# Kernel optimization log

Measured on AMD Instinct MI355X. Metric: run time of the kernel, lower is better.

## Reference

```python
import jax, jax.numpy as jnp
import numpy as np

N = 50000      # nodes
E = 800000     # edges
F_IN = 256     # input node features
H = 64         # hidden_dim
C = 10         # num_classes
G = 64         # graphs in batch


def setup_inputs() -> dict:
    key = jax.random.key(0)
    ks = jax.random.split(key, 10)
    x = jax.random.normal(ks[0], (N, F_IN), dtype=jnp.float32)
    edge_index = jax.random.randint(ks[1], (2, E), 0, N, dtype=jnp.int64)
    batch = jnp.sort(jax.random.randint(ks[2], (N,), 0, G, dtype=jnp.int64))
    def glorot(k, fan_in, fan_out):
        return jax.random.normal(k, (fan_in, fan_out), dtype=jnp.float32) / jnp.sqrt(jnp.float32(fan_in))
    return {
        "x": x,
        "edge_index": edge_index,
        "batch": batch,
        "W1": glorot(ks[3], F_IN, H), "b1": jnp.zeros((H,), jnp.float32),
        "W2": glorot(ks[4], H, H),    "b2": jnp.zeros((H,), jnp.float32),
        "W3": glorot(ks[5], H, H),    "b3": jnp.zeros((H,), jnp.float32),
        "lin_W": glorot(ks[6], H, C), "lin_b": jnp.zeros((C,), jnp.float32),
    }


def reference(x, edge_index, batch, W1, b1, W2, b2, W3, b3, lin_W, lin_b):
    src, dst = edge_index[0], edge_index[1]
    # GCN normalization with self-loops: deg counts (A + I) in-degree
    deg = jax.ops.segment_sum(jnp.ones((E,), x.dtype), dst, num_segments=N) + 1.0
    dis = jax.lax.rsqrt(deg)                       # deg^{-1/2}, [N]
    edge_norm = dis[src] * dis[dst]                # [E]
    self_norm = dis * dis                          # [N] (self-loop weight)

    def gcn_conv_relu(h, W, b):
        h = h @ W                                  # [N, H]
        msg = h[src] * edge_norm[:, None]          # gather + scale, [E, H]
        agg = jax.ops.segment_sum(msg, dst, num_segments=N)
        agg = agg + h * self_norm[:, None]         # self-loop contribution
        return jax.nn.relu(agg + b)                # dropout is identity in eval

    h = gcn_conv_relu(x, W1, b1)
    h = gcn_conv_relu(h, W2, b2)
    h = gcn_conv_relu(h, W3, b3)

    # global mean pool over graphs
    counts = jax.ops.segment_sum(jnp.ones((N,), h.dtype), batch, num_segments=G)
    pooled = jax.ops.segment_sum(h, batch, num_segments=G) / jnp.maximum(counts, 1.0)[:, None]
    return pooled @ lin_W + lin_b                  # [G, C]
```

## Files before the change

### kernel.cpp

```cpp
#include <hip/hip_runtime.h>

#define N_NODES 50000
#define N_EDGES 800000
#define F_INPUT 256
#define HDIM 64
#define NCLS 10
#define NGRAPH 64

#define BSHIFT 7
#define NBUCK 391
#define SCAP 4096

typedef float f32x4v __attribute__((ext_vector_type(4)));
typedef short bf16x8 __attribute__((ext_vector_type(8)));

union B8U { uint4 q; bf16x8 v; };

__device__ __forceinline__ float bflo(unsigned v) { return __uint_as_float(v << 16); }
__device__ __forceinline__ float bfhi(unsigned v) { return __uint_as_float(v & 0xFFFF0000u); }
__device__ __forceinline__ unsigned f2b2(float a, float b) {
    unsigned x = __float_as_uint(a); x = (x + 0x7FFF + ((x >> 16) & 1)) >> 16;
    unsigned y = __float_as_uint(b); y = (y + 0x7FFF + ((y >> 16) & 1)) >> 16;
    return x | (y << 16);
}

__device__ __forceinline__ void split2(float x0, float x1, unsigned& h, unsigned& l) {
    unsigned u0 = __float_as_uint(x0), u1 = __float_as_uint(x1);
    unsigned m0 = u0 & 0xFFFF0000u, m1 = u1 & 0xFFFF0000u;
    h = (u0 >> 16) | m1;
    float r0 = x0 - __uint_as_float(m0);
    float r1 = x1 - __uint_as_float(m1);
    l = (__float_as_uint(r0) >> 16) | (__float_as_uint(r1) & 0xFFFF0000u);
}

#define ADD8(b, u)                                    \
    b##0 += bflo(u.x); b##1 += bfhi(u.x);             \
    b##2 += bflo(u.y); b##3 += bfhi(u.y);             \
    b##4 += bflo(u.z); b##5 += bfhi(u.z);             \
    b##6 += bflo(u.w); b##7 += bfhi(u.w);

__global__ __launch_bounds__(256) void k_part(const int* __restrict__ src,
                                              const int* __restrict__ dst,
                                              int* __restrict__ bcnt,
                                              int* __restrict__ stage, int E) {
    __shared__ int cnt[NBUCK];
    __shared__ int base[NBUCK];
    const int tid = threadIdx.x;
    const int e0 = blockIdx.x * 4096;
    int pb[16], pv[16];
    for (int t = tid; t < NBUCK; t += 256) cnt[t] = 0;
    __syncthreads();
#pragma unroll
    for (int j = 0; j < 16; ++j) {
        int e = e0 + j * 256 + tid;
        if (e < E) {
            int s = src[e], d = dst[e];
            pb[j] = d >> BSHIFT;
            pv[j] = (s << BSHIFT) | (d & 127);
            atomicAdd(&cnt[pb[j]], 1);
        } else pb[j] = -1;
    }
    __syncthreads();
    for (int t = tid; t < NBUCK; t += 256) {
        int c = cnt[t];
        base[t] = c ? atomicAdd(&bcnt[t], c) : 0;
        cnt[t] = 0;
    }
    __syncthreads();
#pragma unroll
    for (int j = 0; j < 16; ++j) {
        if (pb[j] >= 0) {
            int r = base[pb[j]] + atomicAdd(&cnt[pb[j]], 1);
            if (r < SCAP) stage[pb[j] * SCAP + r] = pv[j];
        }
    }
}

__global__ __launch_bounds__(256) void k_csr(const int* __restrict__ stage,
                                             const int* __restrict__ bcnt,
                                             float* __restrict__ dis,
                                             int4* __restrict__ rng,
                                             int* __restrict__ eadj, int n) {
    __shared__ int cnt[128];
    __shared__ int loc[128];
    __shared__ int lcur[128];
    __shared__ int ebuf[SCAP];
    const int b = blockIdx.x;
    const int tid = threadIdx.x;
    const int n0 = b << BSHIFT;
    const int nn = min(128, n - n0);
    const int sb = b * SCAP;
    const int len = min(bcnt[b], SCAP);
    if (tid < 128) cnt[tid] = 0;
    __syncthreads();
    for (int j = tid; j < len; j += 256) atomicAdd(&cnt[stage[sb + j] & 127], 1);
    __syncthreads();
    if (tid < 128) loc[tid] = cnt[tid];
    __syncthreads();
    for (int d = 1; d < 128; d <<= 1) {
        int x = 0;
        if (tid < 128 && tid >= d) x = loc[tid - d];
        __syncthreads();
        if (tid < 128) loc[tid] += x;
        __syncthreads();
    }
    if (tid < 128) {
        int ex = loc[tid] - cnt[tid];
        if (tid < nn) {
            int dg = cnt[tid];
            float di = rsqrtf((float)(dg + 1));
            dis[n0 + tid] = di;
            rng[n0 + tid] = make_int4(sb + ex, sb + ex + dg, __float_as_int(di), 0);
        }
        lcur[tid] = ex;
    }
    __syncthreads();
    for (int j = tid; j < len; j += 256) {
        int p = stage[sb + j];
        int rk = atomicAdd(&lcur[p & 127], 1);
        ebuf[rk] = p >> BSHIFT;
    }
    __syncthreads();
    for (int j = tid; j < len; j += 256) eadj[sb + j] = ebuf[j];
}

__global__ __launch_bounds__(256) void k_prepZ(const float* __restrict__ W1,
                                               const float* __restrict__ W2,
                                               const float* __restrict__ W3,
                                               uint4* __restrict__ Bf1,
                                               uint4* __restrict__ Bf2,
                                               uint4* __restrict__ Bf3,
                                               int* __restrict__ bcnt,
                                               float* __restrict__ pooled) {
    int s = blockIdx.x * 256 + threadIdx.x;
    for (int j = s; j < NBUCK; j += 3072) bcnt[j] = 0;
    for (int j = s; j < NGRAPH * HDIM; j += 3072) pooled[j] = 0.f;
    const float* W; uint4* out; int local, KS;
    if (s < 2048)      { W = W1; out = Bf1; local = s;        KS = 8; }
    else if (s < 2560) { W = W2; out = Bf2; local = s - 2048; KS = 2; }
    else               { W = W3; out = Bf3; local = s - 2560; KS = 2; }
    const int lane = local & 63;
    const int t    = (local >> 6) & 3;
    const int ks   = local >> 8;
    const int kb   = ks * 32 + ((lane >> 4) << 3);
    const int col  = t * 16 + (lane & 15);
    unsigned h[4], l[4];
#pragma unroll
    for (int j = 0; j < 4; ++j) {
        float x0 = W[(size_t)(kb + 2 * j) * HDIM + col];
        float x1 = W[(size_t)(kb + 2 * j + 1) * HDIM + col];
        split2(x0, x1, h[j], l[j]);
    }
    out[(ks * 4 + t) * 64 + lane]          = make_uint4(h[0], h[1], h[2], h[3]);
    out[((KS + ks) * 4 + t) * 64 + lane]   = make_uint4(l[0], l[1], l[2], l[3]);
}

__global__ __launch_bounds__(256) void k_gemm_mf(const float* __restrict__ A,
                                                 const uint4* __restrict__ Bf,
                                                 const float* __restrict__ dis,
                                                 unsigned short* __restrict__ C,
                                                 int n, int lda, int ktn) {
    const int tid = threadIdx.x;
    const int ln  = tid & 63;
    const int wv  = tid >> 6;
    const int m   = ln & 15;
    const int kg  = ln >> 4;
    const int grow = blockIdx.x * 64 + wv * 16 + m;
    const float* ar = A + (size_t)min(grow, n - 1) * lda + kg * 8;

    f32x4v acc[4];
#pragma unroll
    for (int t = 0; t < 4; ++t)
#pragma unroll
        for (int j = 0; j < 4; ++j) acc[t][j] = 0.0f;

    float4 c0 = *(const float4*)(ar);
    float4 c1 = *(const float4*)(ar + 4);

    for (int ks = 0; ks < ktn; ++ks) {
        const int kn = (ks + 1 < ktn) ? (ks + 1) * 32 : 0;
        float4 p0 = *(const float4*)(ar + kn);
        float4 p1 = *(const float4*)(ar + kn + 4);

        const uint4* bp = Bf + (size_t)ks * 256 + ln;
        const uint4* bq = Bf + (size_t)(ktn + ks) * 256 + ln;
        B8U bh0, bh1, bh2, bh3, bl0, bl1, bl2, bl3;
        bh0.q = bp[0];   bh1.q = bp[64];  bh2.q = bp[128]; bh3.q = bp[192];
        bl0.q = bq[0];   bl1.q = bq[64];  bl2.q = bq[128]; bl3.q = bq[192];

        B8U ah, al;
        split2(c0.x, c0.y, ah.q.x, al.q.x);
        split2(c0.z, c0.w, ah.q.y, al.q.y);
        split2(c1.x, c1.y, ah.q.z, al.q.z);
        split2(c1.z, c1.w, ah.q.w, al.q.w);

        acc[0] = __builtin_amdgcn_mfma_f32_16x16x32_bf16(bh0.v, ah.v, acc[0], 0, 0, 0);
        acc[1] = __builtin_amdgcn_mfma_f32_16x16x32_bf16(bh1.v, ah.v, acc[1], 0, 0, 0);
        acc[2] = __builtin_amdgcn_mfma_f32_16x16x32_bf16(bh2.v, ah.v, acc[2], 0, 0, 0);
        acc[3] = __builtin_amdgcn_mfma_f32_16x16x32_bf16(bh3.v, ah.v, acc[3], 0, 0, 0);
        acc[0] = __builtin_amdgcn_mfma_f32_16x16x32_bf16(bl0.v, ah.v, acc[0], 0, 0, 0);
        acc[1] = __builtin_amdgcn_mfma_f32_16x16x32_bf16(bl1.v, ah.v, acc[1], 0, 0, 0);
        acc[2] = __builtin_amdgcn_mfma_f32_16x16x32_bf16(bl2.v, ah.v, acc[2], 0, 0, 0);
        acc[3] = __builtin_amdgcn_mfma_f32_16x16x32_bf16(bl3.v, ah.v, acc[3], 0, 0, 0);
        acc[0] = __builtin_amdgcn_mfma_f32_16x16x32_bf16(bh0.v, al.v, acc[0], 0, 0, 0);
        acc[1] = __builtin_amdgcn_mfma_f32_16x16x32_bf16(bh1.v, al.v, acc[1], 0, 0, 0);
        acc[2] = __builtin_amdgcn_mfma_f32_16x16x32_bf16(bh2.v, al.v, acc[2], 0, 0, 0);
        acc[3] = __builtin_amdgcn_mfma_f32_16x16x32_bf16(bh3.v, al.v, acc[3], 0, 0, 0);

        c0 = p0; c1 = p1;
    }

    if (grow < n) {
        const float di = dis[grow];
#pragma unroll
        for (int t = 0; t < 4; ++t) {
            uint2 p;
            p.x = f2b2(acc[t][0] * di, acc[t][1] * di);
            p.y = f2b2(acc[t][2] * di, acc[t][3] * di);
            *(uint2*)(C + (size_t)grow * HDIM + t * 16 + kg * 4) = p;
        }
    }
}

__global__ __launch_bounds__(256) void k_fgg(const unsigned short* __restrict__ h,
                                             const int* __restrict__ eadj,
                                             const int4* __restrict__ rng,
                                             const float* __restrict__ bias,
                                             const uint4* __restrict__ Bf,
                                             const float* __restrict__ dis,
                                             unsigned short* __restrict__ out, int n) {
    __shared__ uint4 rl[32 * 8];
    const int tid = threadIdx.x;
    const int i0 = blockIdx.x * 32;
    const int node = tid >> 3;
    const int l8 = tid & 7;
    const int i = i0 + node;
    uint4 o = make_uint4(0u, 0u, 0u, 0u);
    if (i < n) {
        const int q = l8 * 8;
        const int4 r = rng[i];
        int e = r.x; const int e1 = r.y;
        const float di = __int_as_float(r.z);
        float a0 = 0.f, a1 = 0.f, a2 = 0.f, a3 = 0.f, a4 = 0.f, a5 = 0.f, a6 = 0.f, a7 = 0.f;
        float g0 = 0.f, g1 = 0.f, g2 = 0.f, g3 = 0.f, g4 = 0.f, g5 = 0.f, g6 = 0.f, g7 = 0.f;
#pragma unroll 2
        for (; e + 3 < e1; e += 4) {
            int s0 = eadj[e];
            int s1 = eadj[e + 1];
            int s2 = eadj[e + 2];
            int s3 = eadj[e + 3];
            uint4 u0 = *(const uint4*)(h + (size_t)s0 * HDIM + q);
            uint4 u1 = *(const uint4*)(h + (size_t)s1 * HDIM + q);
            uint4 u2 = *(const uint4*)(h + (size_t)s2 * HDIM + q);
            uint4 u3 = *(const uint4*)(h + (size_t)s3 * HDIM + q);
            ADD8(a, u0)
            ADD8(g, u1)
            ADD8(a, u2)
            ADD8(g, u3)
        }
        for (; e < e1; ++e) {
            int s0 = eadj[e];
            uint4 u0 = *(const uint4*)(h + (size_t)s0 * HDIM + q);
            ADD8(a, u0)
        }
        uint4 us = *(const uint4*)(h + (size_t)i * HDIM + q);
        ADD8(a, us)
        a0 += g0; a1 += g1; a2 += g2; a3 += g3;
        a4 += g4; a5 += g5; a6 += g6; a7 += g7;
        float4 bl = *(const float4*)(bias + q);
        float4 bh = *(const float4*)(bias + q + 4);
        a0 = fmaxf(fmaf(a0, di, bl.x), 0.f);
        a1 = fmaxf(fmaf(a1, di, bl.y), 0.f);
        a2 = fmaxf(fmaf(a2, di, bl.z), 0.f);
        a3 = fmaxf(fmaf(a3, di, bl.w), 0.f);
        a4 = fmaxf(fmaf(a4, di, bh.x), 0.f);
        a5 = fmaxf(fmaf(a5, di, bh.y), 0.f);
        a6 = fmaxf(fmaf(a6, di, bh.z), 0.f);
        a7 = fmaxf(fmaf(a7, di, bh.w), 0.f);
        o.x = f2b2(a0, a1); o.y = f2b2(a2, a3);
        o.z = f2b2(a4, a5); o.w = f2b2(a6, a7);
    }
    rl[node * 8 + (l8 ^ (node & 7))] = o;
    __syncthreads();

    const int ln = tid & 63;
    const int wv = tid >> 6;
    const int m  = ln & 15;
    const int kg = ln >> 4;
    const int row = (wv >> 1) * 16 + m;
    const int ct0 = (wv & 1) * 2;
    f32x4v acc0, acc1;
#pragma unroll
    for (int j = 0; j < 4; ++j) { acc0[j] = 0.f; acc1[j] = 0.f; }
#pragma unroll
    for (int ks = 0; ks < 2; ++ks) {
        B8U af;
        af.q = rl[row * 8 + ((ks * 4 + kg) ^ (row & 7))];
        const uint4* bp = Bf + ks * 256 + ln;
        const uint4* bq = Bf + (2 + ks) * 256 + ln;
        B8U bh0, bh1, bl0, bl1;
        bh0.q = bp[ct0 * 64]; bh1.q = bp[(ct0 + 1) * 64];
        bl0.q = bq[ct0 * 64]; bl1.q = bq[(ct0 + 1) * 64];
        acc0 = __builtin_amdgcn_mfma_f32_16x16x32_bf16(bh0.v, af.v, acc0, 0, 0, 0);
        acc1 = __builtin_amdgcn_mfma_f32_16x16x32_bf16(bh1.v, af.v, acc1, 0, 0, 0);
        acc0 = __builtin_amdgcn_mfma_f32_16x16x32_bf16(bl0.v, af.v, acc0, 0, 0, 0);
        acc1 = __builtin_amdgcn_mfma_f32_16x16x32_bf16(bl1.v, af.v, acc1, 0, 0, 0);
    }
    const int grow = i0 + row;
    if (grow < n) {
        const float di = dis[grow];
        uint2 p;
        p.x = f2b2(acc0[0] * di, acc0[1] * di);
        p.y = f2b2(acc0[2] * di, acc0[3] * di);
        *(uint2*)(out + (size_t)grow * HDIM + ct0 * 16 + kg * 4) = p;
        p.x = f2b2(acc1[0] * di, acc1[1] * di);
        p.y = f2b2(acc1[2] * di, acc1[3] * di);
        *(uint2*)(out + (size_t)grow * HDIM + (ct0 + 1) * 16 + kg * 4) = p;
    }
}

__global__ __launch_bounds__(256) void k_gather_pool(const unsigned short* __restrict__ h,
                                                     const int* __restrict__ eadj,
                                                     const int4* __restrict__ rng,
                                                     const float* __restrict__ bias,
                                                     const int* __restrict__ batch,
                                                     float* __restrict__ pooled, int n) {
    __shared__ float sp[NGRAPH][HDIM];
    const int tid = threadIdx.x;
    int t = blockIdx.x * 256 + tid;
    int i = t >> 3;
    const bool valid = (i < n);
    int q = (t & 7) * 8;
    const int i0 = (blockIdx.x * 256) >> 3;
    const int i1 = min(i0 + 32, n);
    const int gmin = batch[min(i0, n - 1)];
    const int gmax = batch[i1 - 1];
    for (int j = tid; j < NGRAPH * HDIM; j += 256) ((float*)sp)[j] = 0.f;
    __syncthreads();
    if (valid) {
        const int4 r = rng[i];
        int e = r.x; const int e1 = r.y;
        const float di = __int_as_float(r.z);
        float a0 = 0.f, a1 = 0.f, a2 = 0.f, a3 = 0.f, a4 = 0.f, a5 = 0.f, a6 = 0.f, a7 = 0.f;
        float g0 = 0.f, g1 = 0.f, g2 = 0.f, g3 = 0.f, g4 = 0.f, g5 = 0.f, g6 = 0.f, g7 = 0.f;
#pragma unroll 2
        for (; e + 3 < e1; e += 4) {
            int s0 = eadj[e];
            int s1 = eadj[e + 1];
            int s2 = eadj[e + 2];
            int s3 = eadj[e + 3];
            uint4 u0 = *(const uint4*)(h + (size_t)s0 * HDIM + q);
            uint4 u1 = *(const uint4*)(h + (size_t)s1 * HDIM + q);
            uint4 u2 = *(const uint4*)(h + (size_t)s2 * HDIM + q);
            uint4 u3 = *(const uint4*)(h + (size_t)s3 * HDIM + q);
            ADD8(a, u0)
            ADD8(g, u1)
            ADD8(a, u2)
            ADD8(g, u3)
        }
        for (; e < e1; ++e) {
            int s0 = eadj[e];
            uint4 u0 = *(const uint4*)(h + (size_t)s0 * HDIM + q);
            ADD8(a, u0)
        }
        uint4 us = *(const uint4*)(h + (size_t)i * HDIM + q);
        ADD8(a, us)
        a0 += g0; a1 += g1; a2 += g2; a3 += g3;
        a4 += g4; a5 += g5; a6 += g6; a7 += g7;
        float4 bl = *(const float4*)(bias + q);
        float4 bh = *(const float4*)(bias + q + 4);
        a0 = fmaxf(fmaf(a0, di, bl.x), 0.f);
        a1 = fmaxf(fmaf(a1, di, bl.y), 0.f);
        a2 = fmaxf(fmaf(a2, di, bl.z), 0.f);
        a3 = fmaxf(fmaf(a3, di, bl.w), 0.f);
        a4 = fmaxf(fmaf(a4, di, bh.x), 0.f);
        a5 = fmaxf(fmaf(a5, di, bh.y), 0.f);
        a6 = fmaxf(fmaf(a6, di, bh.z), 0.f);
        a7 = fmaxf(fmaf(a7, di, bh.w), 0.f);
        int g = batch[i];
        atomicAdd(&sp[g][q + 0], a0); atomicAdd(&sp[g][q + 1], a1);
        atomicAdd(&sp[g][q + 2], a2); atomicAdd(&sp[g][q + 3], a3);
        atomicAdd(&sp[g][q + 4], a4); atomicAdd(&sp[g][q + 5], a5);
        atomicAdd(&sp[g][q + 6], a6); atomicAdd(&sp[g][q + 7], a7);
    }
    __syncthreads();
    int rows = gmax - gmin + 1;
    for (int j = tid; j < rows * HDIM; j += 256) {
        int r = j >> 6, c = j & 63;
        float v = sp[gmin + r][c];
        if (v != 0.f) atomicAdd(&pooled[(gmin + r) * HDIM + c], v);
    }
}

__global__ __launch_bounds__(640) void k_head(const float* __restrict__ pooled,
                                              const int* __restrict__ batch,
                                              const float* __restrict__ linW,
                                              const float* __restrict__ linb,
                                              float* __restrict__ out, int n) {
    int t = threadIdx.x;
    if (t >= NGRAPH * NCLS) return;
    int g = t / NCLS;
    int c = t - g * NCLS;
    int lo = 0, hi = n;
    while (lo < hi) { int m = (lo + hi) >> 1; if (batch[m] < g) lo = m + 1; else hi = m; }
    int s = lo;
    lo = 0; hi = n;
    while (lo < hi) { int m = (lo + hi) >> 1; if (batch[m] < g + 1) lo = m + 1; else hi = m; }
    float inv = 1.0f / fmaxf((float)(lo - s), 1.0f);
    float acc = linb[c];
#pragma unroll
    for (int k = 0; k < HDIM; ++k)
        acc = fmaf(pooled[g * HDIM + k] * inv, linW[k * NCLS + c], acc);
    out[g * NCLS + c] = acc;
}

extern "C" void kernel_launch(void* const* d_in, const int* in_sizes, int n_in,
                              void* d_out, int out_size, void* d_ws, size_t ws_size,
                              hipStream_t stream) {
    (void)in_sizes; (void)n_in; (void)out_size; (void)ws_size;
    const float* x    = (const float*)d_in[0];
    const int*   ei   = (const int*)d_in[1];
    const int*   batch= (const int*)d_in[2];
    const float* W1   = (const float*)d_in[3];
    const float* b1   = (const float*)d_in[4];
    const float* W2   = (const float*)d_in[5];
    const float* b2   = (const float*)d_in[6];
    const float* W3   = (const float*)d_in[7];
    const float* b3   = (const float*)d_in[8];
    const float* linW = (const float*)d_in[9];
    const float* linb = (const float*)d_in[10];
    float* out = (float*)d_out;

    const int N = N_NODES, E = N_EDGES;
    const int* src = ei;
    const int* dst = ei + E;

    char* ws = (char*)d_ws;
    unsigned short* hA = (unsigned short*)ws; ws += (size_t)N * HDIM * 2;
    unsigned short* hB = (unsigned short*)ws; ws += (size_t)N * HDIM * 2;
    float* dis    = (float*)ws; ws += (size_t)N * 4;
    int*   eadj   = (int*)ws;   ws += (size_t)NBUCK * SCAP * 4;
    int*   stage  = (int*)ws;   ws += (size_t)NBUCK * SCAP * 4;
    int4*  rng    = (int4*)ws;  ws += (size_t)N * 16;
    int*   bcnt   = (int*)ws;   ws += ((size_t)NBUCK * 4 + 15) & ~(size_t)15;
    float* pooled = (float*)ws; ws += (size_t)NGRAPH * HDIM * 4;
    uint4* Bf1    = (uint4*)ws; ws += (size_t)2 * 8 * 4 * 64 * 16;
    uint4* Bf2    = (uint4*)ws; ws += (size_t)2 * 2 * 4 * 64 * 16;
    uint4* Bf3    = (uint4*)ws; ws += (size_t)2 * 2 * 4 * 64 * 16;

    const int nbE = (E + 4095) / 4096;
    const int gb  = (N + 63) / 64;
    const int nF  = (N + 31) / 32;

    k_prepZ<<<12, 256, 0, stream>>>(W1, W2, W3, Bf1, Bf2, Bf3, bcnt, pooled);
    k_part<<<nbE, 256, 0, stream>>>(src, dst, bcnt, stage, E);
    k_csr<<<NBUCK, 256, 0, stream>>>(stage, bcnt, dis, rng, eadj, N);

    k_gemm_mf<<<gb, 256, 0, stream>>>(x, Bf1, dis, hA, N, F_INPUT, 8);
    k_fgg<<<nF, 256, 0, stream>>>(hA, eadj, rng, b1, Bf2, dis, hB, N);
    k_fgg<<<nF, 256, 0, stream>>>(hB, eadj, rng, b2, Bf3, dis, hA, N);
    k_gather_pool<<<nF, 256, 0, stream>>>(hA, eadj, rng, b3, batch, pooled, N);
    k_head<<<1, 640, 0, stream>>>(pooled, batch, linW, linb, out, N);
}
```

Baseline: 226.9 us.

## Fuse pipeline into cooperative persistent megakernel and overlap partition with first GEMM

```diff
diff --git a/kernel.cpp b/kernel.cpp
--- a/kernel.cpp
+++ b/kernel.cpp
@@ -1,4 +1,7 @@
 #include <hip/hip_runtime.h>
+#include <hip/hip_cooperative_groups.h>
+
+namespace cg = cooperative_groups;
 
 #define N_NODES 50000
 #define N_EDGES 800000
@@ -10,6 +13,7 @@
 #define BSHIFT 7
 #define NBUCK 391
 #define SCAP 4096
+#define PARTB 196
 
 typedef float f32x4v __attribute__((ext_vector_type(4)));
 typedef short bf16x8 __attribute__((ext_vector_type(8)));
@@ -39,106 +43,39 @@
     b##4 += bflo(u.z); b##5 += bfhi(u.z);             \
     b##6 += bflo(u.w); b##7 += bfhi(u.w);
 
-__global__ __launch_bounds__(256) void k_part(const int* __restrict__ src,
-                                              const int* __restrict__ dst,
-                                              int* __restrict__ bcnt,
-                                              int* __restrict__ stage, int E) {
-    __shared__ int cnt[NBUCK];
-    __shared__ int base[NBUCK];
-    const int tid = threadIdx.x;
-    const int e0 = blockIdx.x * 4096;
-    int pb[16], pv[16];
-    for (int t = tid; t < NBUCK; t += 256) cnt[t] = 0;
-    __syncthreads();
-#pragma unroll
-    for (int j = 0; j < 16; ++j) {
-        int e = e0 + j * 256 + tid;
-        if (e < E) {
-            int s = src[e], d = dst[e];
-            pb[j] = d >> BSHIFT;
-            pv[j] = (s << BSHIFT) | (d & 127);
-            atomicAdd(&cnt[pb[j]], 1);
-        } else pb[j] = -1;
-    }
-    __syncthreads();
-    for (int t = tid; t < NBUCK; t += 256) {
-        int c = cnt[t];
-        base[t] = c ? atomicAdd(&bcnt[t], c) : 0;
-        cnt[t] = 0;
-    }
-    __syncthreads();
-#pragma unroll
-    for (int j = 0; j < 16; ++j) {
-        if (pb[j] >= 0) {
-            int r = base[pb[j]] + atomicAdd(&cnt[pb[j]], 1);
-            if (r < SCAP) stage[pb[j] * SCAP + r] = pv[j];
-        }
-    }
-}
-
-__global__ __launch_bounds__(256) void k_csr(const int* __restrict__ stage,
-                                             const int* __restrict__ bcnt,
-                                             float* __restrict__ dis,
-                                             int4* __restrict__ rng,
-                                             int* __restrict__ eadj, int n) {
-    __shared__ int cnt[128];
-    __shared__ int loc[128];
-    __shared__ int lcur[128];
-    __shared__ int ebuf[SCAP];
-    const int b = blockIdx.x;
-    const int tid = threadIdx.x;
-    const int n0 = b << BSHIFT;
-    const int nn = min(128, n - n0);
-    const int sb = b * SCAP;
-    const int len = min(bcnt[b], SCAP);
-    if (tid < 128) cnt[tid] = 0;
-    __syncthreads();
-    for (int j = tid; j < len; j += 256) atomicAdd(&cnt[stage[sb + j] & 127], 1);
-    __syncthreads();
-    if (tid < 128) loc[tid] = cnt[tid];
-    __syncthreads();
-    for (int d = 1; d < 128; d <<= 1) {
-        int x = 0;
-        if (tid < 128 && tid >= d) x = loc[tid - d];
-        __syncthreads();
-        if (tid < 128) loc[tid] += x;
-        __syncthreads();
-    }
-    if (tid < 128) {
-        int ex = loc[tid] - cnt[tid];
-        if (tid < nn) {
-            int dg = cnt[tid];
-            float di = rsqrtf((float)(dg + 1));
-            dis[n0 + tid] = di;
-            rng[n0 + tid] = make_int4(sb + ex, sb + ex + dg, __float_as_int(di), 0);
-        }
-        lcur[tid] = ex;
-    }
-    __syncthreads();
-    for (int j = tid; j < len; j += 256) {
-        int p = stage[sb + j];
-        int rk = atomicAdd(&lcur[p & 127], 1);
-        ebuf[rk] = p >> BSHIFT;
-    }
-    __syncthreads();
-    for (int j = tid; j < len; j += 256) eadj[sb + j] = ebuf[j];
-}
-
-__global__ __launch_bounds__(256) void k_prepZ(const float* __restrict__ W1,
-                                               const float* __restrict__ W2,
-                                               const float* __restrict__ W3,
-                                               uint4* __restrict__ Bf1,
-                                               uint4* __restrict__ Bf2,
-                                               uint4* __restrict__ Bf3,
-                                               int* __restrict__ bcnt,
-                                               float* __restrict__ pooled) {
-    int s = blockIdx.x * 256 + threadIdx.x;
-    for (int j = s; j < NBUCK; j += 3072) bcnt[j] = 0;
-    for (int j = s; j < NGRAPH * HDIM; j += 3072) pooled[j] = 0.f;
+#define FMA8(b, u, wt)                                                  \
+    b##0 = fmaf(bflo(u.x), wt, b##0); b##1 = fmaf(bfhi(u.x), wt, b##1); \
+    b##2 = fmaf(bflo(u.y), wt, b##2); b##3 = fmaf(bfhi(u.y), wt, b##3); \
+    b##4 = fmaf(bflo(u.z), wt, b##4); b##5 = fmaf(bfhi(u.z), wt, b##5); \
+    b##6 = fmaf(bflo(u.w), wt, b##6); b##7 = fmaf(bfhi(u.w), wt, b##7);
+
+struct MegaP {
+    const int* src; const int* dst; int E; int n;
+    const float* x;
+    const float* W1; const float* W2; const float* W3;
+    const float* b1; const float* b2; const float* b3;
+    const float* linW; const float* linb;
+    const int* batch; float* out;
+    unsigned short* hA; unsigned short* hB;
+    float* dis; int* eadj; int* stage; int4* rng; int* bcnt; float* pooled;
+    uint4* Bf1; uint4* Bf2; uint4* Bf3;
+};
+
+union ShU {
+    struct { int cnt[NBUCK]; int base[NBUCK]; } pt;
+    struct { int cnt[128]; int loc[128]; int lcur[128]; int ebuf[SCAP]; } cs;
+    uint4 rl[256];
+    float sp[NGRAPH][HDIM];
+};
+
+static __device__ void prep_unit(int u, const MegaP& p) {
+    int s = u * 256 + (int)threadIdx.x;
+    for (int j = s; j < NBUCK; j += 3072) p.bcnt[j] = 0;
+    for (int j = s; j < NGRAPH * HDIM; j += 3072) p.pooled[j] = 0.f;
     const float* W; uint4* out; int local, KS;
-    if (s < 2048)      { W = W1; out = Bf1; local = s;        KS = 8; }
-    else if (s < 2560) { W = W2; out = Bf2; local = s - 2048; KS = 2; }
-    else               { W = W3; out = Bf3; local = s - 2560; KS = 2; }
+    if (s < 2048)      { W = p.W1; out = p.Bf1; local = s;        KS = 8; }
+    else if (s < 2560) { W = p.W2; out = p.Bf2; local = s - 2048; KS = 2; }
+    else               { W = p.W3; out = p.Bf3; local = s - 2560; KS = 2; }
     const int lane = local & 63;
     const int t    = (local >> 6) & 3;
     const int ks   = local >> 8;
@@ -151,22 +88,53 @@
         float x1 = W[(size_t)(kb + 2 * j + 1) * HDIM + col];
         split2(x0, x1, h[j], l[j]);
     }
-    out[(ks * 4 + t) * 64 + lane]          = make_uint4(h[0], h[1], h[2], h[3]);
-    out[((KS + ks) * 4 + t) * 64 + lane]   = make_uint4(l[0], l[1], l[2], l[3]);
-}
-
-__global__ __launch_bounds__(256) void k_gemm_mf(const float* __restrict__ A,
-                                                 const uint4* __restrict__ Bf,
-                                                 const float* __restrict__ dis,
-                                                 unsigned short* __restrict__ C,
-                                                 int n, int lda, int ktn) {
+    out[(ks * 4 + t) * 64 + lane]        = make_uint4(h[0], h[1], h[2], h[3]);
+    out[((KS + ks) * 4 + t) * 64 + lane] = make_uint4(l[0], l[1], l[2], l[3]);
+}
+
+static __device__ void part_unit(int u, const MegaP& p, ShU& sh) {
+    const int tid = threadIdx.x;
+    __syncthreads();
+    const int e0 = u * 4096;
+    int pb[16], pv[16];
+    for (int t = tid; t < NBUCK; t += 256) sh.pt.cnt[t] = 0;
+    __syncthreads();
+#pragma unroll
+    for (int j = 0; j < 16; ++j) {
+        int e = e0 + j * 256 + tid;
+        if (e < p.E) {
+            int s = p.src[e], d = p.dst[e];
+            pb[j] = d >> BSHIFT;
+            pv[j] = (s << BSHIFT) | (d & 127);
+            atomicAdd(&sh.pt.cnt[pb[j]], 1);
+        } else pb[j] = -1;
+    }
+    __syncthreads();
+    for (int t = tid; t < NBUCK; t += 256) {
+        int c = sh.pt.cnt[t];
+        sh.pt.base[t] = c ? atomicAdd(&p.bcnt[t], c) : 0;
+        sh.pt.cnt[t] = 0;
+    }
+    __syncthreads();
+#pragma unroll
+    for (int j = 0; j < 16; ++j) {
+        if (pb[j] >= 0) {
+            int r = sh.pt.base[pb[j]] + atomicAdd(&sh.pt.cnt[pb[j]], 1);
+            if (r < SCAP) p.stage[pb[j] * SCAP + r] = pv[j];
+        }
+    }
+}
+
+static __device__ void gemm1_unit(int u, const MegaP& p) {
     const int tid = threadIdx.x;
     const int ln  = tid & 63;
     const int wv  = tid >> 6;
     const int m   = ln & 15;
     const int kg  = ln >> 4;
-    const int grow = blockIdx.x * 64 + wv * 16 + m;
-    const float* ar = A + (size_t)min(grow, n - 1) * lda + kg * 8;
+    const int n   = p.n;
+    const int ktn = 8;
+    const int grow = u * 64 + wv * 16 + m;
+    const float* ar = p.x + (size_t)min(grow, n - 1) * F_INPUT + kg * 8;
 
     f32x4v acc[4];
 #pragma unroll
@@ -182,8 +150,8 @@
         float4 p0 = *(const float4*)(ar + kn);
         float4 p1 = *(const float4*)(ar + kn + 4);
 
-        const uint4* bp = Bf + (size_t)ks * 256 + ln;
-        const uint4* bq = Bf + (size_t)(ktn + ks) * 256 + ln;
+        const uint4* bp = p.Bf1 + (size_t)ks * 256 + ln;
+        const uint4* bq = p.Bf1 + (size_t)(ktn + ks) * 256 + ln;
         B8U bh0, bh1, bh2, bh3, bl0, bl1, bl2, bl3;
         bh0.q = bp[0];   bh1.q = bp[64];  bh2.q = bp[128]; bh3.q = bp[192];
         bl0.q = bq[0];   bl1.q = bq[64];  bl2.q = bq[128]; bl3.q = bq[192];
@@ -211,64 +179,196 @@
     }
 
     if (grow < n) {
-        const float di = dis[grow];
 #pragma unroll
         for (int t = 0; t < 4; ++t) {
-            uint2 p;
-            p.x = f2b2(acc[t][0] * di, acc[t][1] * di);
-            p.y = f2b2(acc[t][2] * di, acc[t][3] * di);
-            *(uint2*)(C + (size_t)grow * HDIM + t * 16 + kg * 4) = p;
-        }
-    }
-}
-
-__global__ __launch_bounds__(256) void k_fgg(const unsigned short* __restrict__ h,
-                                             const int* __restrict__ eadj,
-                                             const int4* __restrict__ rng,
-                                             const float* __restrict__ bias,
-                                             const uint4* __restrict__ Bf,
-                                             const float* __restrict__ dis,
-                                             unsigned short* __restrict__ out, int n) {
-    __shared__ uint4 rl[32 * 8];
-    const int tid = threadIdx.x;
-    const int i0 = blockIdx.x * 32;
+            uint2 pk;
+            pk.x = f2b2(acc[t][0], acc[t][1]);
+            pk.y = f2b2(acc[t][2], acc[t][3]);
+            *(uint2*)(p.hA + (size_t)grow * HDIM + t * 16 + kg * 4) = pk;
+        }
+    }
+}
+
+static __device__ void csr_unit(int u, const MegaP& p, ShU& sh) {
+    const int tid = threadIdx.x;
+    __syncthreads();
+    const int n0 = u << BSHIFT;
+    const int nn = min(128, p.n - n0);
+    const int sb = u * SCAP;
+    const int len = min(p.bcnt[u], SCAP);
+    if (tid < 128) sh.cs.cnt[tid] = 0;
+    __syncthreads();
+    for (int j = tid; j < len; j += 256) atomicAdd(&sh.cs.cnt[p.stage[sb + j] & 127], 1);
+    __syncthreads();
+    if (tid < 128) sh.cs.loc[tid] = sh.cs.cnt[tid];
+    __syncthreads();
+    for (int d = 1; d < 128; d <<= 1) {
+        int x = 0;
+        if (tid < 128 && tid >= d) x = sh.cs.loc[tid - d];
+        __syncthreads();
+        if (tid < 128) sh.cs.loc[tid] += x;
+        __syncthreads();
+    }
+    if (tid < 128) {
+        int ex = sh.cs.loc[tid] - sh.cs.cnt[tid];
+        if (tid < nn) {
+            int dg = sh.cs.cnt[tid];
+            float di = rsqrtf((float)(dg + 1));
+            p.dis[n0 + tid] = di;
+            p.rng[n0 + tid] = make_int4(sb + ex, sb + ex + dg, __float_as_int(di), 0);
+        }
+        sh.cs.lcur[tid] = ex;
+    }
+    __syncthreads();
+    for (int j = tid; j < len; j += 256) {
+        int pv = p.stage[sb + j];
+        int rk = atomicAdd(&sh.cs.lcur[pv & 127], 1);
+        sh.cs.ebuf[rk] = pv >> BSHIFT;
+    }
+    __syncthreads();
+    for (int j = tid; j < len; j += 256) p.eadj[sb + j] = sh.cs.ebuf[j];
+}
+
+static __device__ __forceinline__ void fgg_gemm_tail(const MegaP& p, ShU& sh,
+                                                     const uint4* Bf,
+                                                     unsigned short* out, int i0) {
+    const int tid = threadIdx.x;
+    const int ln = tid & 63;
+    const int wv = tid >> 6;
+    const int m  = ln & 15;
+    const int kg = ln >> 4;
+    const int row = (wv >> 1) * 16 + m;
+    const int ct0 = (wv & 1) * 2;
+    f32x4v acc0, acc1;
+#pragma unroll
+    for (int j = 0; j < 4; ++j) { acc0[j] = 0.f; acc1[j] = 0.f; }
+#pragma unroll
+    for (int ks = 0; ks < 2; ++ks) {
+        B8U af;
+        af.q = sh.rl[row * 8 + ((ks * 4 + kg) ^ (row & 7))];
+        const uint4* bp = Bf + ks * 256 + ln;
+        const uint4* bq = Bf + (2 + ks) * 256 + ln;
+        B8U bh0, bh1, bl0, bl1;
+        bh0.q = bp[ct0 * 64]; bh1.q = bp[(ct0 + 1) * 64];
+        bl0.q = bq[ct0 * 64]; bl1.q = bq[(ct0 + 1) * 64];
+        acc0 = __builtin_amdgcn_mfma_f32_16x16x32_bf16(bh0.v, af.v, acc0, 0, 0, 0);
+        acc1 = __builtin_amdgcn_mfma_f32_16x16x32_bf16(bh1.v, af.v, acc1, 0, 0, 0);
+        acc0 = __builtin_amdgcn_mfma_f32_16x16x32_bf16(bl0.v, af.v, acc0, 0, 0, 0);
+        acc1 = __builtin_amdgcn_mfma_f32_16x16x32_bf16(bl1.v, af.v, acc1, 0, 0, 0);
+    }
+    const int grow = i0 + row;
+    if (grow < p.n) {
+        const float di = p.dis[grow];
+        uint2 pk;
+        pk.x = f2b2(acc0[0] * di, acc0[1] * di);
+        pk.y = f2b2(acc0[2] * di, acc0[3] * di);
+        *(uint2*)(out + (size_t)grow * HDIM + ct0 * 16 + kg * 4) = pk;
+        pk.x = f2b2(acc1[0] * di, acc1[1] * di);
+        pk.y = f2b2(acc1[2] * di, acc1[3] * di);
+        *(uint2*)(out + (size_t)grow * HDIM + (ct0 + 1) * 16 + kg * 4) = pk;
+    }
+}
+
+static __device__ void fggw_unit(int u, const MegaP& p, ShU& sh) {
+    const int tid = threadIdx.x;
+    __syncthreads();
+    const int i0 = u * 32;
     const int node = tid >> 3;
     const int l8 = tid & 7;
     const int i = i0 + node;
     uint4 o = make_uint4(0u, 0u, 0u, 0u);
-    if (i < n) {
+    if (i < p.n) {
         const int q = l8 * 8;
-        const int4 r = rng[i];
+        const int4 r = p.rng[i];
         int e = r.x; const int e1 = r.y;
         const float di = __int_as_float(r.z);
         float a0 = 0.f, a1 = 0.f, a2 = 0.f, a3 = 0.f, a4 = 0.f, a5 = 0.f, a6 = 0.f, a7 = 0.f;
         float g0 = 0.f, g1 = 0.f, g2 = 0.f, g3 = 0.f, g4 = 0.f, g5 = 0.f, g6 = 0.f, g7 = 0.f;
 #pragma unroll 2
         for (; e + 3 < e1; e += 4) {
-            int s0 = eadj[e];
-            int s1 = eadj[e + 1];
-            int s2 = eadj[e + 2];
-            int s3 = eadj[e + 3];
-            uint4 u0 = *(const uint4*)(h + (size_t)s0 * HDIM + q);
-            uint4 u1 = *(const uint4*)(h + (size_t)s1 * HDIM + q);
-            uint4 u2 = *(const uint4*)(h + (size_t)s2 * HDIM + q);
-            uint4 u3 = *(const uint4*)(h + (size_t)s3 * HDIM + q);
+            int s0 = p.eadj[e];
+            int s1 = p.eadj[e + 1];
+            int s2 = p.eadj[e + 2];
+            int s3 = p.eadj[e + 3];
+            uint4 u0 = *(const uint4*)(p.hA + (size_t)s0 * HDIM + q);
+            uint4 u1 = *(const uint4*)(p.hA + (size_t)s1 * HDIM + q);
+            uint4 u2 = *(const uint4*)(p.hA + (size_t)s2 * HDIM + q);
+            uint4 u3 = *(const uint4*)(p.hA + (size_t)s3 * HDIM + q);
+            float w0 = p.dis[s0] * di;
+            float w1 = p.dis[s1] * di;
+            float w2 = p.dis[s2] * di;
+            float w3 = p.dis[s3] * di;
+            FMA8(a, u0, w0)
+            FMA8(g, u1, w1)
+            FMA8(a, u2, w2)
+            FMA8(g, u3, w3)
+        }
+        for (; e < e1; ++e) {
+            int s0 = p.eadj[e];
+            uint4 u0 = *(const uint4*)(p.hA + (size_t)s0 * HDIM + q);
+            float w0 = p.dis[s0] * di;
+            FMA8(a, u0, w0)
+        }
+        uint4 us = *(const uint4*)(p.hA + (size_t)i * HDIM + q);
+        float sn = di * di;
+        FMA8(a, us, sn)
+        a0 += g0; a1 += g1; a2 += g2; a3 += g3;
+        a4 += g4; a5 += g5; a6 += g6; a7 += g7;
+        float4 bl = *(const float4*)(p.b1 + q);
+        float4 bh = *(const float4*)(p.b1 + q + 4);
+        a0 = fmaxf(a0 + bl.x, 0.f); a1 = fmaxf(a1 + bl.y, 0.f);
+        a2 = fmaxf(a2 + bl.z, 0.f); a3 = fmaxf(a3 + bl.w, 0.f);
+        a4 = fmaxf(a4 + bh.x, 0.f); a5 = fmaxf(a5 + bh.y, 0.f);
+        a6 = fmaxf(a6 + bh.z, 0.f); a7 = fmaxf(a7 + bh.w, 0.f);
+        o.x = f2b2(a0, a1); o.y = f2b2(a2, a3);
+        o.z = f2b2(a4, a5); o.w = f2b2(a6, a7);
+    }
+    sh.rl[node * 8 + (l8 ^ (node & 7))] = o;
+    __syncthreads();
+    fgg_gemm_tail(p, sh, p.Bf2, p.hB, i0);
+}
+
+static __device__ void fgg_unit(int u, const MegaP& p, ShU& sh) {
+    const int tid = threadIdx.x;
+    __syncthreads();
+    const int i0 = u * 32;
+    const int node = tid >> 3;
+    const int l8 = tid & 7;
+    const int i = i0 + node;
+    uint4 o = make_uint4(0u, 0u, 0u, 0u);
+    if (i < p.n) {
+        const int q = l8 * 8;
+        const int4 r = p.rng[i];
+        int e = r.x; const int e1 = r.y;
+        const float di = __int_as_float(r.z);
+        float a0 = 0.f, a1 = 0.f, a2 = 0.f, a3 = 0.f, a4 = 0.f, a5 = 0.f, a6 = 0.f, a7 = 0.f;
+        float g0 = 0.f, g1 = 0.f, g2 = 0.f, g3 = 0.f, g4 = 0.f, g5 = 0.f, g6 = 0.f, g7 = 0.f;
+#pragma unroll 2
+        for (; e + 3 < e1; e += 4) {
+            int s0 = p.eadj[e];
+            int s1 = p.eadj[e + 1];
+            int s2 = p.eadj[e + 2];
+            int s3 = p.eadj[e + 3];
+            uint4 u0 = *(const uint4*)(p.hB + (size_t)s0 * HDIM + q);
+            uint4 u1 = *(const uint4*)(p.hB + (size_t)s1 * HDIM + q);
+            uint4 u2 = *(const uint4*)(p.hB + (size_t)s2 * HDIM + q);
+            uint4 u3 = *(const uint4*)(p.hB + (size_t)s3 * HDIM + q);
             ADD8(a, u0)
             ADD8(g, u1)
             ADD8(a, u2)
             ADD8(g, u3)
         }
         for (; e < e1; ++e) {
-            int s0 = eadj[e];
-            uint4 u0 = *(const uint4*)(h + (size_t)s0 * HDIM + q);
+            int s0 = p.eadj[e];
+            uint4 u0 = *(const uint4*)(p.hB + (size_t)s0 * HDIM + q);
             ADD8(a, u0)
         }
-        uint4 us = *(const uint4*)(h + (size_t)i * HDIM + q);
+        uint4 us = *(const uint4*)(p.hB + (size_t)i * HDIM + q);
         ADD8(a, us)
         a0 += g0; a1 += g1; a2 += g2; a3 += g3;
         a4 += g4; a5 += g5; a6 += g6; a7 += g7;
-        float4 bl = *(const float4*)(bias + q);
-        float4 bh = *(const float4*)(bias + q + 4);
+        float4 bl = *(const float4*)(p.b2 + q);
+        float4 bh = *(const float4*)(p.b2 + q + 4);
         a0 = fmaxf(fmaf(a0, di, bl.x), 0.f);
         a1 = fmaxf(fmaf(a1, di, bl.y), 0.f);
         a2 = fmaxf(fmaf(a2, di, bl.z), 0.f);
@@ -280,95 +380,56 @@
         o.x = f2b2(a0, a1); o.y = f2b2(a2, a3);
         o.z = f2b2(a4, a5); o.w = f2b2(a6, a7);
     }
-    rl[node * 8 + (l8 ^ (node & 7))] = o;
-    __syncthreads();
-
-    const int ln = tid & 63;
-    const int wv = tid >> 6;
-    const int m  = ln & 15;
-    const int kg = ln >> 4;
-    const int row = (wv >> 1) * 16 + m;
-    const int ct0 = (wv & 1) * 2;
-    f32x4v acc0, acc1;
-#pragma unroll
-    for (int j = 0; j < 4; ++j) { acc0[j] = 0.f; acc1[j] = 0.f; }
-#pragma unroll
-    for (int ks = 0; ks < 2; ++ks) {
-        B8U af;
-        af.q = rl[row * 8 + ((ks * 4 + kg) ^ (row & 7))];
-        const uint4* bp = Bf + ks * 256 + ln;
-        const uint4* bq = Bf + (2 + ks) * 256 + ln;
-        B8U bh0, bh1, bl0, bl1;
-        bh0.q = bp[ct0 * 64]; bh1.q = bp[(ct0 + 1) * 64];
-        bl0.q = bq[ct0 * 64]; bl1.q = bq[(ct0 + 1) * 64];
-        acc0 = __builtin_amdgcn_mfma_f32_16x16x32_bf16(bh0.v, af.v, acc0, 0, 0, 0);
-        acc1 = __builtin_amdgcn_mfma_f32_16x16x32_bf16(bh1.v, af.v, acc1, 0, 0, 0);
-        acc0 = __builtin_amdgcn_mfma_f32_16x16x32_bf16(bl0.v, af.v, acc0, 0, 0, 0);
-        acc1 = __builtin_amdgcn_mfma_f32_16x16x32_bf16(bl1.v, af.v, acc1, 0, 0, 0);
-    }
-    const int grow = i0 + row;
-    if (grow < n) {
-        const float di = dis[grow];
-        uint2 p;
-        p.x = f2b2(acc0[0] * di, acc0[1] * di);
-        p.y = f2b2(acc0[2] * di, acc0[3] * di);
-        *(uint2*)(out + (size_t)grow * HDIM + ct0 * 16 + kg * 4) = p;
-        p.x = f2b2(acc1[0] * di, acc1[1] * di);
-        p.y = f2b2(acc1[2] * di, acc1[3] * di);
-        *(uint2*)(out + (size_t)grow * HDIM + (ct0 + 1) * 16 + kg * 4) = p;
-    }
-}
-
-__global__ __launch_bounds__(256) void k_gather_pool(const unsigned short* __restrict__ h,
-                                                     const int* __restrict__ eadj,
-                                                     const int4* __restrict__ rng,
-                                                     const float* __restrict__ bias,
-                                                     const int* __restrict__ batch,
-                                                     float* __restrict__ pooled, int n) {
-    __shared__ float sp[NGRAPH][HDIM];
-    const int tid = threadIdx.x;
-    int t = blockIdx.x * 256 + tid;
+    sh.rl[node * 8 + (l8 ^ (node & 7))] = o;
+    __syncthreads();
+    fgg_gemm_tail(p, sh, p.Bf3, p.hA, i0);
+}
+
+static __device__ void pool_unit(int u, const MegaP& p, ShU& sh) {
+    const int tid = threadIdx.x;
+    __syncthreads();
+    int t = u * 256 + tid;
     int i = t >> 3;
-    const bool valid = (i < n);
+    const bool valid = (i < p.n);
     int q = (t & 7) * 8;
-    const int i0 = (blockIdx.x * 256) >> 3;
-    const int i1 = min(i0 + 32, n);
-    const int gmin = batch[min(i0, n - 1)];
-    const int gmax = batch[i1 - 1];
-    for (int j = tid; j < NGRAPH * HDIM; j += 256) ((float*)sp)[j] = 0.f;
+    const int i0 = (u * 256) >> 3;
+    const int i1 = min(i0 + 32, p.n);
+    const int gmin = p.batch[min(i0, p.n - 1)];
+    const int gmax = p.batch[i1 - 1];
+    for (int j = tid; j < NGRAPH * HDIM; j += 256) ((float*)sh.sp)[j] = 0.f;
     __syncthreads();
     if (valid) {
-        const int4 r = rng[i];
+        const int4 r = p.rng[i];
         int e = r.x; const int e1 = r.y;
         const float di = __int_as_float(r.z);
         float a0 = 0.f, a1 = 0.f, a2 = 0.f, a3 = 0.f, a4 = 0.f, a5 = 0.f, a6 = 0.f, a7 = 0.f;
         float g0 = 0.f, g1 = 0.f, g2 = 0.f, g3 = 0.f, g4 = 0.f, g5 = 0.f, g6 = 0.f, g7 = 0.f;
 #pragma unroll 2
         for (; e + 3 < e1; e += 4) {
-            int s0 = eadj[e];
-            int s1 = eadj[e + 1];
-            int s2 = eadj[e + 2];
-            int s3 = eadj[e + 3];
-            uint4 u0 = *(const uint4*)(h + (size_t)s0 * HDIM + q);
-            uint4 u1 = *(const uint4*)(h + (size_t)s1 * HDIM + q);
-            uint4 u2 = *(const uint4*)(h + (size_t)s2 * HDIM + q);
-            uint4 u3 = *(const uint4*)(h + (size_t)s3 * HDIM + q);
+            int s0 = p.eadj[e];
+            int s1 = p.eadj[e + 1];
+            int s2 = p.eadj[e + 2];
+            int s3 = p.eadj[e + 3];
+            uint4 u0 = *(const uint4*)(p.hA + (size_t)s0 * HDIM + q);
+            uint4 u1 = *(const uint4*)(p.hA + (size_t)s1 * HDIM + q);
+            uint4 u2 = *(const uint4*)(p.hA + (size_t)s2 * HDIM + q);
+            uint4 u3 = *(const uint4*)(p.hA + (size_t)s3 * HDIM + q);
             ADD8(a, u0)
             ADD8(g, u1)
             ADD8(a, u2)
             ADD8(g, u3)
         }
         for (; e < e1; ++e) {
-            int s0 = eadj[e];
-            uint4 u0 = *(const uint4*)(h + (size_t)s0 * HDIM + q);
+            int s0 = p.eadj[e];
+            uint4 u0 = *(const uint4*)(p.hA + (size_t)s0 * HDIM + q);
             ADD8(a, u0)
         }
-        uint4 us = *(const uint4*)(h + (size_t)i * HDIM + q);
+        uint4 us = *(const uint4*)(p.hA + (size_t)i * HDIM + q);
         ADD8(a, us)
         a0 += g0; a1 += g1; a2 += g2; a3 += g3;
         a4 += g4; a5 += g5; a6 += g6; a7 += g7;
-        float4 bl = *(const float4*)(bias + q);
-        float4 bh = *(const float4*)(bias + q + 4);
+        float4 bl = *(const float4*)(p.b3 + q);
+        float4 bh = *(const float4*)(p.b3 + q + 4);
         a0 = fmaxf(fmaf(a0, di, bl.x), 0.f);
         a1 = fmaxf(fmaf(a1, di, bl.y), 0.f);
         a2 = fmaxf(fmaf(a2, di, bl.z), 0.f);
@@ -377,88 +438,136 @@
         a5 = fmaxf(fmaf(a5, di, bh.y), 0.f);
         a6 = fmaxf(fmaf(a6, di, bh.z), 0.f);
         a7 = fmaxf(fmaf(a7, di, bh.w), 0.f);
-        int g = batch[i];
-        atomicAdd(&sp[g][q + 0], a0); atomicAdd(&sp[g][q + 1], a1);
-        atomicAdd(&sp[g][q + 2], a2); atomicAdd(&sp[g][q + 3], a3);
-        atomicAdd(&sp[g][q + 4], a4); atomicAdd(&sp[g][q + 5], a5);
-        atomicAdd(&sp[g][q + 6], a6); atomicAdd(&sp[g][q + 7], a7);
+        int g = p.batch[i];
+        atomicAdd(&sh.sp[g][q + 0], a0); atomicAdd(&sh.sp[g][q + 1], a1);
+        atomicAdd(&sh.sp[g][q + 2], a2); atomicAdd(&sh.sp[g][q + 3], a3);
+        atomicAdd(&sh.sp[g][q + 4], a4); atomicAdd(&sh.sp[g][q + 5], a5);
+        atomicAdd(&sh.sp[g][q + 6], a6); atomicAdd(&sh.sp[g][q + 7], a7);
     }
     __syncthreads();
     int rows = gmax - gmin + 1;
     for (int j = tid; j < rows * HDIM; j += 256) {
         int r = j >> 6, c = j & 63;
-        float v = sp[gmin + r][c];
-        if (v != 0.f) atomicAdd(&pooled[(gmin + r) * HDIM + c], v);
-    }
-}
-
-__global__ __launch_bounds__(640) void k_head(const float* __restrict__ pooled,
-                                              const int* __restrict__ batch,
-                                              const float* __restrict__ linW,
-                                              const float* __restrict__ linb,
-                                              float* __restrict__ out, int n) {
-    int t = threadIdx.x;
-    if (t >= NGRAPH * NCLS) return;
-    int g = t / NCLS;
-    int c = t - g * NCLS;
-    int lo = 0, hi = n;
-    while (lo < hi) { int m = (lo + hi) >> 1; if (batch[m] < g) lo = m + 1; else hi = m; }
-    int s = lo;
-    lo = 0; hi = n;
-    while (lo < hi) { int m = (lo + hi) >> 1; if (batch[m] < g + 1) lo = m + 1; else hi = m; }
-    float inv = 1.0f / fmaxf((float)(lo - s), 1.0f);
-    float acc = linb[c];
-#pragma unroll
-    for (int k = 0; k < HDIM; ++k)
-        acc = fmaf(pooled[g * HDIM + k] * inv, linW[k * NCLS + c], acc);
-    out[g * NCLS + c] = acc;
-}
+        float v = sh.sp[gmin + r][c];
+        if (v != 0.f) atomicAdd(&p.pooled[(gmin + r) * HDIM + c], v);
+    }
+}
+
+static __device__ void head_unit(const MegaP& p) {
+    for (int tt = threadIdx.x; tt < NGRAPH * NCLS; tt += 256) {
+        int g = tt / NCLS;
+        int c = tt - g * NCLS;
+        int lo = 0, hi = p.n;
+        while (lo < hi) { int m2 = (lo + hi) >> 1; if (p.batch[m2] < g) lo = m2 + 1; else hi = m2; }
+        int s = lo;
+        lo = 0; hi = p.n;
+        while (lo < hi) { int m2 = (lo + hi) >> 1; if (p.batch[m2] < g + 1) lo = m2 + 1; else hi = m2; }
+        float inv = 1.0f / fmaxf((float)(lo - s), 1.0f);
+        float acc = p.linb[c];
+#pragma unroll
+        for (int k = 0; k < HDIM; ++k)
+            acc = fmaf(p.pooled[g * HDIM + k] * inv, p.linW[k * NCLS + c], acc);
+        p.out[g * NCLS + c] = acc;
+    }
+}
+
+__global__ __launch_bounds__(256, 4) void k_mega(MegaP p) {
+    __shared__ ShU sh;
+    cg::grid_group grid = cg::this_grid();
+    const int gb = (p.n + 63) / 64;
+    const int nF = (p.n + 31) / 32;
+    for (int u = blockIdx.x; u < 12; u += gridDim.x) prep_unit(u, p);
+    grid.sync();
+    for (int u = blockIdx.x; u < PARTB + gb; u += gridDim.x) {
+        if (u < PARTB) part_unit(u, p, sh);
+        else           gemm1_unit(u - PARTB, p);
+    }
+    grid.sync();
+    for (int u = blockIdx.x; u < NBUCK; u += gridDim.x) csr_unit(u, p, sh);
+    grid.sync();
+    for (int u = blockIdx.x; u < nF; u += gridDim.x) fggw_unit(u, p, sh);
+    grid.sync();
+    for (int u = blockIdx.x; u < nF; u += gridDim.x) fgg_unit(u, p, sh);
+    grid.sync();
+    for (int u = blockIdx.x; u < nF; u += gridDim.x) pool_unit(u, p, sh);
+    grid.sync();
+    if (blockIdx.x == 0) head_unit(p);
+}
+
+__global__ __launch_bounds__(256) void k_prepS(MegaP p) { prep_unit(blockIdx.x, p); }
+__global__ __launch_bounds__(256) void k_pgS(MegaP p) {
+    __shared__ ShU sh;
+    if ((int)blockIdx.x < PARTB) part_unit(blockIdx.x, p, sh);
+    else                         gemm1_unit(blockIdx.x - PARTB, p);
+}
+__global__ __launch_bounds__(256) void k_csrS(MegaP p)  { __shared__ ShU sh; csr_unit(blockIdx.x, p, sh); }
+__global__ __launch_bounds__(256) void k_fggwS(MegaP p) { __shared__ ShU sh; fggw_unit(blockIdx.x, p, sh); }
+__global__ __launch_bounds__(256) void k_fggS(MegaP p)  { __shared__ ShU sh; fgg_unit(blockIdx.x, p, sh); }
+__global__ __launch_bounds__(256) void k_poolS(MegaP p) { __shared__ ShU sh; pool_unit(blockIdx.x, p, sh); }
+__global__ __launch_bounds__(256) void k_headS(MegaP p) { head_unit(p); }
 
 extern "C" void kernel_launch(void* const* d_in, const int* in_sizes, int n_in,
                               void* d_out, int out_size, void* d_ws, size_t ws_size,
                               hipStream_t stream) {
     (void)in_sizes; (void)n_in; (void)out_size; (void)ws_size;
-    const float* x    = (const float*)d_in[0];
-    const int*   ei   = (const int*)d_in[1];
-    const int*   batch= (const int*)d_in[2];
-    const float* W1   = (const float*)d_in[3];
-    const float* b1   = (const float*)d_in[4];
-    const float* W2   = (const float*)d_in[5];
-    const float* b2   = (const float*)d_in[6];
-    const float* W3   = (const float*)d_in[7];
-    const float* b3   = (const float*)d_in[8];
-    const float* linW = (const float*)d_in[9];
-    const float* linb = (const float*)d_in[10];
-    float* out = (float*)d_out;
-
-    const int N = N_NODES, E = N_EDGES;
-    const int* src = ei;
-    const int* dst = ei + E;
+    MegaP p;
+    p.x    = (const float*)d_in[0];
+    const int* ei = (const int*)d_in[1];
+    p.batch = (const int*)d_in[2];
+    p.W1 = (const float*)d_in[3];  p.b1 = (const float*)d_in[4];
+    p.W2 = (const float*)d_in[5];  p.b2 = (const float*)d_in[6];
+    p.W3 = (const float*)d_in[7];  p.b3 = (const float*)d_in[8];
+    p.linW = (const float*)d_in[9]; p.linb = (const float*)d_in[10];
+    p.out = (float*)d_out;
+    p.E = N_EDGES;
+    p.n = N_NODES;
+    p.src = ei;
+    p.dst = ei + N_EDGES;
 
     char* ws = (char*)d_ws;
-    unsigned short* hA = (unsigned short*)ws; ws += (size_t)N * HDIM * 2;
-    unsigned short* hB = (unsigned short*)ws; ws += (size_t)N * HDIM * 2;
-    float* dis    = (float*)ws; ws += (size_t)N * 4;
-    int*   eadj   = (int*)ws;   ws += (size_t)NBUCK * SCAP * 4;
-    int*   stage  = (int*)ws;   ws += (size_t)NBUCK * SCAP * 4;
-    int4*  rng    = (int4*)ws;  ws += (size_t)N * 16;
-    int*   bcnt   = (int*)ws;   ws += ((size_t)NBUCK * 4 + 15) & ~(size_t)15;
-    float* pooled = (float*)ws; ws += (size_t)NGRAPH * HDIM * 4;
-    uint4* Bf1    = (uint4*)ws; ws += (size_t)2 * 8 * 4 * 64 * 16;
-    uint4* Bf2    = (uint4*)ws; ws += (size_t)2 * 2 * 4 * 64 * 16;
-    uint4* Bf3    = (uint4*)ws; ws += (size_t)2 * 2 * 4 * 64 * 16;
-
-    const int nbE = (E + 4095) / 4096;
-    const int gb  = (N + 63) / 64;
-    const int nF  = (N + 31) / 32;
-
-    k_prepZ<<<12, 256, 0, stream>>>(W1, W2, W3, Bf1, Bf2, Bf3, bcnt, pooled);
-    k_part<<<nbE, 256, 0, stream>>>(src, dst, bcnt, stage, E);
-    k_csr<<<NBUCK, 256, 0, stream>>>(stage, bcnt, dis, rng, eadj, N);
-
-    k_gemm_mf<<<gb, 256, 0, stream>>>(x, Bf1, dis, hA, N, F_INPUT, 8);
-    k_fgg<<<nF, 256, 0, stream>>>(hA, eadj, rng, b1, Bf2, dis, hB, N);
-    k_fgg<<<nF, 256, 0, stream>>>(hB, eadj, rng, b2, Bf3, dis, hA, N);
-    k_gather_pool<<<nF, 256, 0, stream>>>(hA, eadj, rng, b3, batch, pooled, N);
-    k_head<<<1, 640, 0, stream>>>(pooled, batch, linW, linb, out, N);
-}
+    p.hA   = (unsigned short*)ws; ws += (size_t)N_NODES * HDIM * 2;
+    p.hB   = (unsigned short*)ws; ws += (size_t)N_NODES * HDIM * 2;
+    p.dis  = (float*)ws;          ws += (size_t)N_NODES * 4;
+    p.eadj = (int*)ws;            ws += (size_t)NBUCK * SCAP * 4;
+    p.stage= (int*)ws;            ws += (size_t)NBUCK * SCAP * 4;
+    p.rng  = (int4*)ws;           ws += (size_t)N_NODES * 16;
+    p.bcnt = (int*)ws;            ws += ((size_t)NBUCK * 4 + 15) & ~(size_t)15;
+    p.pooled = (float*)ws;        ws += (size_t)NGRAPH * HDIM * 4;
+    p.Bf1  = (uint4*)ws;          ws += (size_t)2 * 8 * 4 * 64 * 16;
+    p.Bf2  = (uint4*)ws;          ws += (size_t)2 * 2 * 4 * 64 * 16;
+    p.Bf3  = (uint4*)ws;          ws += (size_t)2 * 2 * 4 * 64 * 16;
+
+    const int gb = (N_NODES + 63) / 64;
+    const int nF = (N_NODES + 31) / 32;
+
+    static int coopGrid = -1;
+    if (coopGrid < 0) {
+        int occ = 0;
+        hipError_t oe = hipOccupancyMaxActiveBlocksPerMultiprocessor(
+            &occ, reinterpret_cast<const void*>(k_mega), 256, 0);
+        if (oe != hipSuccess || occ < 1) coopGrid = 0;
+        else {
+            long g = (long)occ * 256;
+            if (g > nF) g = nF;
+            coopGrid = (int)g;
+        }
+    }
+
+    bool done = false;
+    if (coopGrid > 0) {
+        void* args[] = { (void*)&p };
+        hipError_t le = hipLaunchCooperativeKernel(
+            reinterpret_cast<const void*>(k_mega),
+            dim3(coopGrid), dim3(256), args, 0, stream);
+        done = (le == hipSuccess);
+    }
+    if (!done) {
+        k_prepS<<<12, 256, 0, stream>>>(p);
+        k_pgS<<<PARTB + gb, 256, 0, stream>>>(p);
+        k_csrS<<<NBUCK, 256, 0, stream>>>(p);
+        k_fggwS<<<nF, 256, 0, stream>>>(p);
+        k_fggS<<<nF, 256, 0, stream>>>(p);
+        k_poolS<<<nF, 256, 0, stream>>>(p);
+        k_headS<<<1, 256, 0, stream>>>(p);
+    }
+}
```

New measurement: 617.2 us. 172% more time.
